# Optimization experiments

Measured on AMD Instinct MI355X. Metric: run time of the kernel, lower is better.

The kernel has to match this reference:

```python
import jax, jax.numpy as jnp
import numpy as np
import math

D_MODEL = 1024
H = 16
D_K = D_MODEL // H
D_FF = 4096
EPS = 1e-6


def layer_norm(x, gamma, beta):
    # torch LayerNorm-variant: unbiased std, eps added to std (not var)
    mean = jnp.mean(x, axis=-1, keepdims=True)
    std = jnp.std(x, axis=-1, keepdims=True, ddof=1)
    return gamma * (x - mean) / (std + EPS) + beta


def mha(x, mask, w_q, w_k, w_v, w_o):
    B, S, _ = x.shape
    # torch Linear (no bias): y = x @ W.T
    q = (x @ w_q.T).reshape(B, S, H, D_K).transpose(0, 2, 1, 3)
    k = (x @ w_k.T).reshape(B, S, H, D_K).transpose(0, 2, 1, 3)
    v = (x @ w_v.T).reshape(B, S, H, D_K).transpose(0, 2, 1, 3)
    scores = jnp.einsum('bhqd,bhkd->bhqk', q, k) / math.sqrt(D_K)
    scores = jnp.where(mask == 0, jnp.float32(-1e9), scores)
    attn = jax.nn.softmax(scores, axis=-1)
    out = jnp.einsum('bhqk,bhkd->bhqd', attn, v)
    out = out.transpose(0, 2, 1, 3).reshape(B, S, D_MODEL)
    return out @ w_o.T


def setup_inputs() -> dict:
    key = jax.random.key(0)
    ks = jax.random.split(key, 12)
    B, S = 4, 2048
    s = 0.02
    return {
        'x': jax.random.normal(ks[0], (B, S, D_MODEL), jnp.float32),
        'src_mask': jnp.ones((B, 1, 1, S), jnp.int32),
        'w_q': jax.random.normal(ks[1], (D_MODEL, D_MODEL), jnp.float32) * s,
        'w_k': jax.random.normal(ks[2], (D_MODEL, D_MODEL), jnp.float32) * s,
        'w_v': jax.random.normal(ks[3], (D_MODEL, D_MODEL), jnp.float32) * s,
        'w_o': jax.random.normal(ks[4], (D_MODEL, D_MODEL), jnp.float32) * s,
        'w1': jax.random.normal(ks[5], (D_FF, D_MODEL), jnp.float32) * s,
        'b1': jnp.zeros((D_FF,), jnp.float32),
        'w2': jax.random.normal(ks[6], (D_MODEL, D_FF), jnp.float32) * s,
        'b2': jnp.zeros((D_MODEL,), jnp.float32),
        'gamma1': jnp.ones((D_MODEL,), jnp.float32),
        'beta1': jnp.zeros((D_MODEL,), jnp.float32),
        'gamma2': jnp.ones((D_MODEL,), jnp.float32),
        'beta2': jnp.zeros((D_MODEL,), jnp.float32),
    }


def reference(x, src_mask, w_q, w_k, w_v, w_o, w1, b1, w2, b2,
              gamma1, beta1, gamma2, beta2):
    # AddNorm1: x + MHA(LN(x))  (pre-norm, dropout=0)
    x = x + mha(layer_norm(x, gamma1, beta1), src_mask, w_q, w_k, w_v, w_o)
    # AddNorm2: x + FFN(LN(x))
    h = layer_norm(x, gamma2, beta2)
    ffn = jax.nn.relu(h @ w1.T + b1) @ w2.T + b2
    return x + ffn
```

## Files before the change

kernel.cpp:

```cpp
#include <hip/hip_runtime.h>

#define D_MODEL 1024
#define NH 16
#define DK 64
#define DFF 4096
#define SEQ 2048
#define BATCH 4
#define NROWS (BATCH*SEQ)
#define CHUNK 2048
#define NCHUNK (NROWS/CHUNK)

typedef short bf16x8 __attribute__((ext_vector_type(8)));
typedef float f32x4 __attribute__((ext_vector_type(4)));

__device__ __forceinline__ float bf2f(unsigned short u){
  union { float f; unsigned int i; } x; x.i = ((unsigned int)u) << 16; return x.f;
}
__device__ __forceinline__ unsigned short f2bf(float f){
  union { float f; unsigned int i; } x; x.f = f;
  unsigned int r = x.i + 0x7fffu + ((x.i >> 16) & 1u);
  return (unsigned short)(r >> 16);
}
__device__ __forceinline__ float fexp2(float x){
#if __has_builtin(__builtin_amdgcn_exp2f)
  return __builtin_amdgcn_exp2f(x);
#else
  return __exp2f(x);
#endif
}

__device__ __forceinline__ void gl_lds16(const void* g, void* l) {
  __builtin_amdgcn_global_load_lds((const __attribute__((address_space(1))) void*)g,
                                   (__attribute__((address_space(3))) void*)l, 16, 0, 0);
}

__device__ __forceinline__ int xcd_swz(int hid, int total) {
  return (hid & 7) * (total >> 3) + (hid >> 3);
}

__global__ __launch_bounds__(256) void cvt_f2b(const float* __restrict__ in,
                                               unsigned short* __restrict__ out, int n)
{
  int i = (blockIdx.x * 256 + threadIdx.x) * 4;
  if (i < n) {
    float4 f = *(const float4*)(in + i);
    union { int2 v; unsigned short u[4]; } o;
    o.u[0] = f2bf(f.x); o.u[1] = f2bf(f.y); o.u[2] = f2bf(f.z); o.u[3] = f2bf(f.w);
    *(int2*)(out + i) = o.v;
  }
}

__global__ __launch_bounds__(256) void ln_kernel(const float* __restrict__ in,
    const float* __restrict__ gam, const float* __restrict__ bet,
    unsigned short* __restrict__ out)
{
  const int row = blockIdx.x, t = threadIdx.x;
  const int base = t * 4;
  float4 raw = *(const float4*)(in + (size_t)row * D_MODEL + base);
  float v[4] = { raw.x, raw.y, raw.z, raw.w };
  float s  = v[0] + v[1] + v[2] + v[3];
  float s2 = v[0]*v[0] + v[1]*v[1] + v[2]*v[2] + v[3]*v[3];
  #pragma unroll
  for (int off = 32; off > 0; off >>= 1) {
    s  += __shfl_down(s,  off);
    s2 += __shfl_down(s2, off);
  }
  __shared__ float red[10];
  const int wid = t >> 6, lane = t & 63;
  if (lane == 0) { red[wid] = s; red[4 + wid] = s2; }
  __syncthreads();
  if (t == 0) {
    float ts  = red[0] + red[1] + red[2] + red[3];
    float ts2 = red[4] + red[5] + red[6] + red[7];
    float mean = ts * (1.0f / D_MODEL);
    float var  = (ts2 - (float)D_MODEL * mean * mean) * (1.0f / (D_MODEL - 1));
    var = fmaxf(var, 0.0f);
    red[8] = mean;
    red[9] = 1.0f / (sqrtf(var) + 1e-6f);
  }
  __syncthreads();
  const float mean = red[8], inv = red[9];
  float4 g4 = *(const float4*)(gam + base);
  float4 b4 = *(const float4*)(bet + base);
  union { int2 v; unsigned short u[4]; } o;
  o.u[0] = f2bf(g4.x * (v[0] - mean) * inv + b4.x);
  o.u[1] = f2bf(g4.y * (v[1] - mean) * inv + b4.y);
  o.u[2] = f2bf(g4.z * (v[2] - mean) * inv + b4.z);
  o.u[3] = f2bf(g4.w * (v[3] - mean) * inv + b4.w);
  *(int2*)(out + (size_t)row * D_MODEL + base) = o.v;
}

__global__ __launch_bounds__(256, 4) void gemm_bt(
    const unsigned short* __restrict__ A,
    const unsigned short* __restrict__ Bw,
    int K, int N, int sA, int sB,
    const float* __restrict__ bias,
    int relu,
    const float* __restrict__ residf,
    unsigned short* __restrict__ outb,
    float* __restrict__ outf,
    float* __restrict__ atomf,
    unsigned short* __restrict__ outq,
    unsigned short* __restrict__ outk,
    unsigned short* __restrict__ outvt)
{
  __shared__ __attribute__((aligned(16))) short sA0[128 * 32];
  __shared__ __attribute__((aligned(16))) short sA1[128 * 32];
  __shared__ __attribute__((aligned(16))) short sB0[128 * 32];
  __shared__ __attribute__((aligned(16))) short sB1[128 * 32];
  const int t = threadIdx.x;
  const int lid  = xcd_swz(blockIdx.y * gridDim.x + blockIdx.x,
                           gridDim.x * gridDim.y);
  const int tileN = (lid % gridDim.x) * 128;
  const int tileM = (lid / gridDim.x) * 128;
  const int kz = blockIdx.z;
  const size_t koff = (size_t)kz * K;
  const int wid = t >> 6, lane = t & 63;
  const int wM = (wid >> 1) * 64, wN = (wid & 1) * 64;
  const int quad = lane >> 4, lrow = lane & 15;

  f32x4 acc[4][4] = {};

  const int slotg = ((t & 3) ^ ((t >> 3) & 3)) * 8;
  const unsigned short* pa = A  + (size_t)(tileM + (t >> 2)) * sA + koff + slotg;
  const unsigned short* pb = Bw + (size_t)(tileN + (t >> 2)) * sB + koff + slotg;
  const size_t a64 = (size_t)64 * sA, b64 = (size_t)64 * sB;

  auto stageTo = [&](short* dA, short* dB) {
    gl_lds16(pa,       dA + t * 8);
    gl_lds16(pa + a64, dA + (256 + t) * 8);
    gl_lds16(pb,       dB + t * 8);
    gl_lds16(pb + b64, dB + (256 + t) * 8);
    pa += 32; pb += 32;
  };
  const int sq = (quad ^ ((lrow >> 1) & 3)) * 8;
  auto compute = [&](const short* cA, const short* cB) {
    bf16x8 af[4], bfr[4];
    #pragma unroll
    for (int i = 0; i < 4; i++) {
      af[i]  = *(const bf16x8*)&cA[(wM + i * 16 + lrow) * 32 + sq];
      bfr[i] = *(const bf16x8*)&cB[(wN + i * 16 + lrow) * 32 + sq];
    }
    #pragma unroll
    for (int i = 0; i < 4; i++)
      #pragma unroll
      for (int j = 0; j < 4; j++)
        acc[i][j] = __builtin_amdgcn_mfma_f32_16x16x32_bf16(af[i], bfr[j], acc[i][j], 0, 0, 0);
  };

  const int nk = K >> 5;
  stageTo(sA0, sB0);
  __syncthreads();
  for (int ik = 0; ik < nk; ik += 2) {
    if (ik + 1 < nk) stageTo(sA1, sB1);
    compute(sA0, sB0);
    __syncthreads();
    if (ik + 2 < nk) stageTo(sA0, sB0);
    compute(sA1, sB1);
    __syncthreads();
  }

  unsigned short* qk_out = nullptr;
  int qkv_cat = 0;
  if (outq) {
    qkv_cat = tileN >> 10;
    qk_out = (qkv_cat == 0) ? outq : outk;
  }

  #pragma unroll
  for (int i = 0; i < 4; i++) {
    #pragma unroll
    for (int j = 0; j < 4; j++) {
      const int col  = tileN + wN + j * 16 + lrow;
      const int row0 = tileM + wM + i * 16 + quad * 4;
      const float bv = (bias && kz == 0) ? bias[col] : 0.0f;
      float vals[4];
      #pragma unroll
      for (int r = 0; r < 4; r++) {
        float val = acc[i][j][r] + bv;
        if (relu) val = fmaxf(val, 0.0f);
        if (residf) val += residf[(size_t)(row0 + r) * N + col];
        vals[r] = val;
      }
      if (outq) {
        const int lcol = col & 1023;
        if (qkv_cat < 2) {
          #pragma unroll
          for (int r = 0; r < 4; r++)
            qk_out[(size_t)(row0 + r) * D_MODEL + lcol] = f2bf(vals[r]);
        } else {
          union { int2 v; unsigned short u[4]; } pk;
          #pragma unroll
          for (int r = 0; r < 4; r++) pk.u[r] = f2bf(vals[r]);
          size_t tidx = (((size_t)(row0 >> 11) * NH + (lcol >> 6)) * DK + (lcol & 63)) * SEQ + (row0 & 2047);
          *(int2*)(outvt + tidx) = pk.v;
        }
      } else if (atomf) {
        #pragma unroll
        for (int r = 0; r < 4; r++)
          atomicAdd(&atomf[(size_t)(row0 + r) * N + col], vals[r]);
      } else {
        #pragma unroll
        for (int r = 0; r < 4; r++) {
          const size_t idx = (size_t)(row0 + r) * N + col;
          if (outf) outf[idx] = vals[r];
          if (outb) outb[idx] = f2bf(vals[r]);
        }
      }
    }
  }
}

#define AQT 128
#define AKT 64
__global__ __launch_bounds__(256) void attn_mfma(
    const unsigned short* __restrict__ Qg,
    const unsigned short* __restrict__ Kg,
    const unsigned short* __restrict__ Vt,
    const int* __restrict__ mask,
    unsigned short* __restrict__ Og)
{
  __shared__ __attribute__((aligned(16))) short Ks[AKT * 64];
  __shared__ __attribute__((aligned(16))) short Vs[DK * 64];
  __shared__ __attribute__((aligned(16))) short Ps0[64 * 64];
  __shared__ __attribute__((aligned(16))) short Ps1[64 * 64];
  __shared__ __attribute__((aligned(16))) float maddf[AKT];

  const int bid = xcd_swz(blockIdx.x, gridDim.x);
  const int nqt = SEQ / AQT;
  const int b  = bid / (NH * nqt);
  const int h  = (bid / nqt) % NH;
  const int q0 = (bid % nqt) * AQT;
  const int t  = threadIdx.x;
  const int wv = t >> 6, lane = t & 63;
  const int quad = lane >> 4, l15 = lane & 15;
  const int sw = (l15 & 7) << 3;
  const float SCL = 0.125f * 1.44269504f;

  bf16x8 qf[2][2];
  #pragma unroll
  for (int g = 0; g < 2; g++) {
    const unsigned short* qrow =
        Qg + (size_t)(b * SEQ + q0 + g * 64 + wv * 16 + l15) * D_MODEL + h * DK;
    qf[g][0] = *(const bf16x8*)(qrow + quad * 8);
    qf[g][1] = *(const bf16x8*)(qrow + 32 + quad * 8);
  }
  f32x4 oacc[2][4] = {};
  float m_run[2] = { -1e30f, -1e30f };
  float l_run[2] = { 0.0f, 0.0f };

  const int srow = t >> 3;
  const int scol = ((t & 7) * 8) ^ ((srow & 7) << 3);
  const unsigned short* kp = Kg + (size_t)(b * SEQ + srow) * D_MODEL + h * DK + scol;
  const unsigned short* vp = Vt + ((size_t)(b * NH + h) * DK + srow) * SEQ + scol;
  const int* mp = mask + b * SEQ;
  const int prow = wv * 16 + l15;

  for (int kt = 0; kt < SEQ; kt += AKT) {
    gl_lds16(kp,                  &Ks[t * 8]);
    gl_lds16(kp + 32 * D_MODEL,   &Ks[(256 + t) * 8]);
    gl_lds16(vp,                  &Vs[t * 8]);
    gl_lds16(vp + 32 * SEQ,       &Vs[(256 + t) * 8]);
    if (t < AKT) maddf[t] = mp[t] ? 0.0f : -1.0e9f;
    __syncthreads();

    f32x4 sc[2][4];
    #pragma unroll
    for (int ct = 0; ct < 4; ct++) {
      const int krow = ct * 16 + l15;
      bf16x8 kb0 = *(const bf16x8*)&Ks[krow * 64 + ((quad * 8) ^ sw)];
      bf16x8 kb1 = *(const bf16x8*)&Ks[krow * 64 + ((32 + quad * 8) ^ sw)];
      f32x4 a0 = {}, a1 = {};
      a0 = __builtin_amdgcn_mfma_f32_16x16x32_bf16(kb0, qf[0][0], a0, 0, 0, 0);
      a0 = __builtin_amdgcn_mfma_f32_16x16x32_bf16(kb1, qf[0][1], a0, 0, 0, 0);
      a1 = __builtin_amdgcn_mfma_f32_16x16x32_bf16(kb0, qf[1][0], a1, 0, 0, 0);
      a1 = __builtin_amdgcn_mfma_f32_16x16x32_bf16(kb1, qf[1][1], a1, 0, 0, 0);
      f32x4 md = *(const f32x4*)&maddf[ct * 16 + quad * 4];
      #pragma unroll
      for (int r = 0; r < 4; r++) {
        a0[r] = a0[r] * SCL + md[r];
        a1[r] = a1[r] * SCL + md[r];
      }
      sc[0][ct] = a0; sc[1][ct] = a1;
    }

    #pragma unroll
    for (int g = 0; g < 2; g++) {
      short* Pg = g ? Ps1 : Ps0;
      float tmax = fmaxf(fmaxf(sc[g][0][0], sc[g][0][1]), fmaxf(sc[g][0][2], sc[g][0][3]));
      #pragma unroll
      for (int ct = 1; ct < 4; ct++)
        tmax = fmaxf(tmax, fmaxf(fmaxf(sc[g][ct][0], sc[g][ct][1]),
                                 fmaxf(sc[g][ct][2], sc[g][ct][3])));
      tmax = fmaxf(tmax, __shfl_xor(tmax, 16));
      tmax = fmaxf(tmax, __shfl_xor(tmax, 32));

      if (!__all(tmax - m_run[g] <= 11.5415603f)) {
        float mn = fmaxf(m_run[g], tmax);
        float alpha = fexp2(m_run[g] - mn);
        m_run[g] = mn;
        l_run[g] *= alpha;
        float a4[4];
        #pragma unroll
        for (int r = 0; r < 4; r++) a4[r] = __shfl(alpha, quad * 4 + r);
        #pragma unroll
        for (int dt = 0; dt < 4; dt++)
          #pragma unroll
          for (int r = 0; r < 4; r++) oacc[g][dt][r] *= a4[r];
      }

      float rs = 0.0f;
      #pragma unroll
      for (int ct = 0; ct < 4; ct++) {
        float p0 = fexp2(sc[g][ct][0] - m_run[g]);
        float p1 = fexp2(sc[g][ct][1] - m_run[g]);
        float p2 = fexp2(sc[g][ct][2] - m_run[g]);
        float p3 = fexp2(sc[g][ct][3] - m_run[g]);
        rs += (p0 + p1) + (p2 + p3);
        unsigned int lo, hi;
        asm("v_cvt_pk_bf16_f32 %0, %1, %2" : "=v"(lo) : "v"(p0), "v"(p1));
        asm("v_cvt_pk_bf16_f32 %0, %1, %2" : "=v"(hi) : "v"(p2), "v"(p3));
        int2 pv; pv.x = (int)lo; pv.y = (int)hi;
        *(int2*)&Pg[prow * 64 + ((ct * 16 + quad * 4) ^ sw)] = pv;
      }
      rs += __shfl_xor(rs, 16);
      rs += __shfl_xor(rs, 32);
      l_run[g] += rs;
    }

    bf16x8 pf00 = *(const bf16x8*)&Ps0[prow * 64 + ((quad * 8) ^ sw)];
    bf16x8 pf01 = *(const bf16x8*)&Ps0[prow * 64 + ((32 + quad * 8) ^ sw)];
    bf16x8 pf10 = *(const bf16x8*)&Ps1[prow * 64 + ((quad * 8) ^ sw)];
    bf16x8 pf11 = *(const bf16x8*)&Ps1[prow * 64 + ((32 + quad * 8) ^ sw)];
    #pragma unroll
    for (int dt = 0; dt < 4; dt++) {
      const int vrow = dt * 16 + l15;
      bf16x8 vb0 = *(const bf16x8*)&Vs[vrow * 64 + ((quad * 8) ^ sw)];
      bf16x8 vb1 = *(const bf16x8*)&Vs[vrow * 64 + ((32 + quad * 8) ^ sw)];
      oacc[0][dt] = __builtin_amdgcn_mfma_f32_16x16x32_bf16(pf00, vb0, oacc[0][dt], 0, 0, 0);
      oacc[0][dt] = __builtin_amdgcn_mfma_f32_16x16x32_bf16(pf01, vb1, oacc[0][dt], 0, 0, 0);
      oacc[1][dt] = __builtin_amdgcn_mfma_f32_16x16x32_bf16(pf10, vb0, oacc[1][dt], 0, 0, 0);
      oacc[1][dt] = __builtin_amdgcn_mfma_f32_16x16x32_bf16(pf11, vb1, oacc[1][dt], 0, 0, 0);
    }
    __syncthreads();
    kp += (size_t)AKT * D_MODEL; vp += AKT; mp += AKT;
  }

  #pragma unroll
  for (int g = 0; g < 2; g++) {
    float li = 1.0f / l_run[g];
    float linv4[4];
    #pragma unroll
    for (int r = 0; r < 4; r++) linv4[r] = __shfl(li, quad * 4 + r);
    #pragma unroll
    for (int dt = 0; dt < 4; dt++)
      #pragma unroll
      for (int r = 0; r < 4; r++)
        Og[(size_t)(b * SEQ + q0 + g * 64 + wv * 16 + quad * 4 + r) * D_MODEL + h * DK + dt * 16 + l15] =
          f2bf(oacc[g][dt][r] * linv4[r]);
  }
}

extern "C" void kernel_launch(void* const* d_in, const int* in_sizes, int n_in,
                              void* d_out, int out_size, void* d_ws, size_t ws_size,
                              hipStream_t stream)
{
  (void)in_sizes; (void)n_in; (void)out_size; (void)ws_size;
  const float* x   = (const float*)d_in[0];
  const int*   msk = (const int*)d_in[1];
  const float* w_q = (const float*)d_in[2];
  const float* w_k = (const float*)d_in[3];
  const float* w_v = (const float*)d_in[4];
  const float* w_o = (const float*)d_in[5];
  const float* w1  = (const float*)d_in[6];
  const float* b1  = (const float*)d_in[7];
  const float* w2  = (const float*)d_in[8];
  const float* b2  = (const float*)d_in[9];
  const float* g1  = (const float*)d_in[10];
  const float* be1 = (const float*)d_in[11];
  const float* g2  = (const float*)d_in[12];
  const float* be2 = (const float*)d_in[13];
  float* outf = (float*)d_out;

  char* ws = (char*)d_ws;
  const size_t MB = 1024 * 1024;
  unsigned short* q_b  = (unsigned short*)(ws + 0);
  unsigned short* k_b  = (unsigned short*)(ws + 16 * MB);
  unsigned short* vt_b = (unsigned short*)(ws + 32 * MB);
  unsigned short* wo16 = (unsigned short*)(ws + 16 * MB);
  unsigned short* w116 = (unsigned short*)(ws + 0);
  unsigned short* w216 = (unsigned short*)(ws + 8 * MB);
  unsigned short* ln2b = vt_b;
  unsigned short* hffc = k_b;

  unsigned short* ln1b   = (unsigned short*)d_out;
  unsigned short* wqkv16 = (unsigned short*)d_out + 8 * 1024 * 1024;

  dim3 blk(256);
  const int nw = D_MODEL * D_MODEL;
  const int nf = DFF * D_MODEL;

  cvt_f2b<<<nw / 1024, blk, 0, stream>>>(w_q, wqkv16, nw);
  cvt_f2b<<<nw / 1024, blk, 0, stream>>>(w_k, wqkv16 + nw, nw);
  cvt_f2b<<<nw / 1024, blk, 0, stream>>>(w_v, wqkv16 + 2 * nw, nw);
  ln_kernel<<<NROWS, blk, 0, stream>>>(x, g1, be1, ln1b);

  dim3 gqkv(3 * D_MODEL / 128, NROWS / 128);
  gemm_bt<<<gqkv, blk, 0, stream>>>(ln1b, wqkv16, D_MODEL, 3 * D_MODEL, D_MODEL, D_MODEL,
                                    nullptr, 0, nullptr, nullptr, nullptr, nullptr,
                                    q_b, k_b, vt_b);

  attn_mfma<<<BATCH * NH * (SEQ / AQT), blk, 0, stream>>>(q_b, k_b, vt_b, msk, q_b);

  cvt_f2b<<<nw / 1024, blk, 0, stream>>>(w_o, wo16, nw);
  dim3 gN1024(D_MODEL / 128, NROWS / 128);
  gemm_bt<<<gN1024, blk, 0, stream>>>(q_b, wo16, D_MODEL, D_MODEL, D_MODEL, D_MODEL,
                                      nullptr, 0, x, nullptr, outf, nullptr,
                                      nullptr, nullptr, nullptr);

  cvt_f2b<<<nf / 1024, blk, 0, stream>>>(w1, w116, nf);
  cvt_f2b<<<nf / 1024, blk, 0, stream>>>(w2, w216, nf);
  ln_kernel<<<NROWS, blk, 0, stream>>>(outf, g2, be2, ln2b);
  for (int c = 0; c < NCHUNK; c++) {
    const size_t ro = (size_t)c * CHUNK;
    dim3 g1c(DFF / 128,     CHUNK / 128);
    dim3 g2c(D_MODEL / 128, CHUNK / 128, 4);
    gemm_bt<<<g1c, blk, 0, stream>>>(ln2b + ro * D_MODEL, w116, D_MODEL, DFF,
                                     D_MODEL, D_MODEL, b1, 1,
                                     nullptr, hffc, nullptr, nullptr,
                                     nullptr, nullptr, nullptr);
    gemm_bt<<<g2c, blk, 0, stream>>>(hffc, w216, DFF / 4, D_MODEL, DFF, DFF, b2, 0,
                                     nullptr, nullptr, nullptr, outf + ro * D_MODEL,
                                     nullptr, nullptr, nullptr);
  }
}
```

Before: 693.1 us.

## Triple-buffer GEMM LDS staging with explicit vmcnt waits instead of syncthreads

The bf16 GEMM moves from a double-buffered to a triple-buffered LDS pipeline. It keeps two k-steps of global_load_lds in flight and waits with s_waitcnt vmcnt(8) plus raw s_barrier instead of a full __syncthreads drain. The goal is to hide global load latency behind MFMA compute. In exchange it uses 50% more LDS, lowers the launch-bounds occupancy hint from 4 to 3 blocks, and issues redundant clamped loads at the tail.

```diff
diff --git a/kernel.cpp b/kernel.cpp
--- a/kernel.cpp
+++ b/kernel.cpp
@@ -32,6 +32,15 @@
 __device__ __forceinline__ void gl_lds16(const void* g, void* l) {
   __builtin_amdgcn_global_load_lds((const __attribute__((address_space(1))) void*)g,
                                    (__attribute__((address_space(3))) void*)l, 16, 0, 0);
+}
+
+__device__ __forceinline__ void vwait8() {
+  asm volatile("s_waitcnt vmcnt(8)" ::: "memory");
+  __builtin_amdgcn_sched_barrier(0);
+}
+__device__ __forceinline__ void vwait0() {
+  asm volatile("s_waitcnt vmcnt(0)" ::: "memory");
+  __builtin_amdgcn_sched_barrier(0);
 }
 
 __device__ __forceinline__ int xcd_swz(int hid, int total) {
@@ -90,7 +99,7 @@
   *(int2*)(out + (size_t)row * D_MODEL + base) = o.v;
 }
 
-__global__ __launch_bounds__(256, 4) void gemm_bt(
+__global__ __launch_bounds__(256, 3) void gemm_bt(
     const unsigned short* __restrict__ A,
     const unsigned short* __restrict__ Bw,
     int K, int N, int sA, int sB,
@@ -106,8 +115,10 @@
 {
   __shared__ __attribute__((aligned(16))) short sA0[128 * 32];
   __shared__ __attribute__((aligned(16))) short sA1[128 * 32];
+  __shared__ __attribute__((aligned(16))) short sA2[128 * 32];
   __shared__ __attribute__((aligned(16))) short sB0[128 * 32];
   __shared__ __attribute__((aligned(16))) short sB1[128 * 32];
+  __shared__ __attribute__((aligned(16))) short sB2[128 * 32];
   const int t = threadIdx.x;
   const int lid  = xcd_swz(blockIdx.y * gridDim.x + blockIdx.x,
                            gridDim.x * gridDim.y);
@@ -126,12 +137,13 @@
   const unsigned short* pb = Bw + (size_t)(tileN + (t >> 2)) * sB + koff + slotg;
   const size_t a64 = (size_t)64 * sA, b64 = (size_t)64 * sB;
 
-  auto stageTo = [&](short* dA, short* dB) {
-    gl_lds16(pa,       dA + t * 8);
-    gl_lds16(pa + a64, dA + (256 + t) * 8);
-    gl_lds16(pb,       dB + t * 8);
-    gl_lds16(pb + b64, dB + (256 + t) * 8);
-    pa += 32; pb += 32;
+  auto stageTo = [&](short* dA, short* dB, int kstep) {
+    const unsigned short* qa = pa + (kstep << 5);
+    const unsigned short* qb = pb + (kstep << 5);
+    gl_lds16(qa,       dA + t * 8);
+    gl_lds16(qa + a64, dA + (256 + t) * 8);
+    gl_lds16(qb,       dB + t * 8);
+    gl_lds16(qb + b64, dB + (256 + t) * 8);
   };
   const int sq = (quad ^ ((lrow >> 1) & 3)) * 8;
   auto compute = [&](const short* cA, const short* cB) {
@@ -149,16 +161,28 @@
   };
 
   const int nk = K >> 5;
-  stageTo(sA0, sB0);
-  __syncthreads();
-  for (int ik = 0; ik < nk; ik += 2) {
-    if (ik + 1 < nk) stageTo(sA1, sB1);
+  stageTo(sA0, sB0, 0);
+  stageTo(sA1, sB1, 1);
+  stageTo(sA2, sB2, 2);
+  for (int ik = 0; ik < nk; ik += 3) {
+    vwait8(); __builtin_amdgcn_s_barrier();
     compute(sA0, sB0);
-    __syncthreads();
-    if (ik + 2 < nk) stageTo(sA0, sB0);
-    compute(sA1, sB1);
-    __syncthreads();
-  }
+    __builtin_amdgcn_s_barrier();
+    { int kn = ik + 3; if (kn > nk - 1) kn = nk - 1; stageTo(sA0, sB0, kn); }
+    if (ik + 1 < nk) {
+      vwait8(); __builtin_amdgcn_s_barrier();
+      compute(sA1, sB1);
+      __builtin_amdgcn_s_barrier();
+      int kn = ik + 4; if (kn > nk - 1) kn = nk - 1; stageTo(sA1, sB1, kn);
+    }
+    if (ik + 2 < nk) {
+      vwait8(); __builtin_amdgcn_s_barrier();
+      compute(sA2, sB2);
+      __builtin_amdgcn_s_barrier();
+      int kn = ik + 5; if (kn > nk - 1) kn = nk - 1; stageTo(sA2, sB2, kn);
+    }
+  }
+  vwait0();
 
   unsigned short* qk_out = nullptr;
   int qkv_cat = 0;
```

Measured after the change: 695.3 us. No clear change (+0.3%).
